# Optimization experiments

Hardware: AMD Instinct MI355X
Metric: run time of the kernel (lower is better)

The kernel has to match this reference:

```python
import jax, jax.numpy as jnp
import numpy as np

N_DET, N_MAP, N_PTS, C = 900, 100, 20, 256
IMG_W, IMG_H = 640.0, 480.0


def _grid_sample(feat, gx, gy):
    """Bilinear grid_sample, align_corners=False, zeros padding.
    feat: [C,H,W]; gx,gy: [N] normalized in [-1,1]. Returns [N,C]."""
    Cc, H, W = feat.shape
    x = (gx + 1.0) * (W * 0.5) - 0.5
    y = (gy + 1.0) * (H * 0.5) - 0.5
    x0 = jnp.floor(x); y0 = jnp.floor(y)
    wx1 = x - x0; wx0 = 1.0 - wx1
    wy1 = y - y0; wy0 = 1.0 - wy1

    def gather(xi, yi):
        inb = (xi >= 0) & (xi <= W - 1) & (yi >= 0) & (yi <= H - 1)
        xc = jnp.clip(xi, 0, W - 1).astype(jnp.int32)
        yc = jnp.clip(yi, 0, H - 1).astype(jnp.int32)
        return feat[:, yc, xc] * inb.astype(feat.dtype)  # [C,N]

    out = (gather(x0, y0) * (wx0 * wy0) + gather(x0 + 1, y0) * (wx1 * wy0)
           + gather(x0, y0 + 1) * (wx0 * wy1) + gather(x0 + 1, y0 + 1) * (wx1 * wy1))
    return out.T  # [N,C]


def _project(E, K, homo):
    """E:[6,4,4], K:[6,3,3], homo:[N,4] -> gx,gy,valid each [6,N]."""
    pc = jnp.einsum('cij,nj->cni', E, homo)            # [6,N,4]
    p2d = jnp.einsum('cij,cnj->cni', K, pc[..., :3])   # [6,N,3]
    depth = p2d[..., 2]
    u = p2d[..., 0] / (depth + 1e-6)
    v = p2d[..., 1] / (depth + 1e-6)
    valid = depth > 0.1
    gx = u / IMG_W * 2.0 - 1.0
    gy = v / IMG_H * 2.0 - 1.0
    return gx, gy, valid


def _sample_multiscale(feats, gx, gy, valid):
    """feats: list of [6,C,H,W]; gx,gy,valid: [6,N] -> [6,N,C]."""
    acc = None
    for f in feats:  # fixed 4 FPN levels
        s = jax.vmap(_grid_sample)(f, gx, gy)  # [6,N,C]
        acc = s if acc is None else acc + s
    acc = acc / len(feats)
    return acc * valid[..., None].astype(acc.dtype)


def setup_inputs():
    key = jax.random.key(0)
    ks = jax.random.split(key, 16)
    f = lambda i, shape, s=1.0: jax.random.normal(ks[i], shape, jnp.float32) * s
    p2 = f(0, (6, C, 120, 160))
    p3 = f(1, (6, C, 60, 80))
    p4 = f(2, (6, C, 30, 40))
    p5 = f(3, (6, C, 15, 20))
    K0 = jnp.array([[500.0, 0.0, 320.0], [0.0, 500.0, 240.0], [0.0, 0.0, 1.0]], jnp.float32)
    intrinsics = jnp.tile(K0, (6, 1, 1)) + f(4, (6, 3, 3), 0.5)
    extrinsics = jnp.tile(jnp.eye(4, dtype=jnp.float32), (6, 1, 1)) + f(5, (6, 4, 4), 0.3)
    det_anchors_3d = f(6, (N_DET, 3), 20.0)
    det_anchors_full = f(7, (N_DET, 11))
    map_anchors = f(8, (N_MAP, N_PTS, 2), 20.0)
    s = 1.0 / float(np.sqrt(C))
    return {
        'p2': p2, 'p3': p3, 'p4': p4, 'p5': p5,
        'intrinsics': intrinsics, 'extrinsics': extrinsics,
        'det_anchors_3d': det_anchors_3d, 'det_anchors_full': det_anchors_full,
        'map_anchors': map_anchors,
        'W1d': f(9, (C, C), s), 'b1d': jnp.zeros((C,), jnp.float32),
        'Wcd': f(10, (C, 4), s), 'bcd': jnp.zeros((4,), jnp.float32),
        'Wod': f(11, (C, 11), s), 'bod': jnp.zeros((11,), jnp.float32),
        'W1m': f(12, (C, C), s), 'b1m': jnp.zeros((C,), jnp.float32),
        'Wcm': f(13, (C, 3), s), 'bcm': jnp.zeros((3,), jnp.float32),
        'Wom': f(14, (C, N_PTS * 2), s), 'bom': jnp.zeros((N_PTS * 2,), jnp.float32),
    }


def reference(p2, p3, p4, p5, intrinsics, extrinsics, det_anchors_3d,
              det_anchors_full, map_anchors, W1d, b1d, Wcd, bcd, Wod, bod,
              W1m, b1m, Wcm, bcm, Wom, bom):
    feats = [p2, p3, p4, p5]
    ones_det = jnp.ones((N_DET, 1), det_anchors_3d.dtype)
    homo_det = jnp.concatenate([det_anchors_3d, ones_det], axis=-1)  # [900,4]
    centers = map_anchors.mean(axis=1)  # [100,2]
    homo_map = jnp.concatenate([centers,
                                jnp.zeros((N_MAP, 1), centers.dtype),
                                jnp.ones((N_MAP, 1), centers.dtype)], axis=-1)  # [100,4]

    gxd, gyd, vd = _project(extrinsics, intrinsics, homo_det)
    det_agg = _sample_multiscale(feats, gxd, gyd, vd).sum(0) / 6.0  # [900,256]
    gxm, gym, vm = _project(extrinsics, intrinsics, homo_map)
    map_agg = _sample_multiscale(feats, gxm, gym, vm).sum(0) / 6.0  # [100,256]

    hd = jax.nn.relu(det_agg @ W1d + b1d)
    det_classes = hd @ Wcd + bcd                     # [900,4]
    det_boxes = det_anchors_full + hd @ Wod + bod    # [900,11]
    hm = jax.nn.relu(map_agg @ W1m + b1m)
    map_classes = hm @ Wcm + bcm                     # [100,3]
    map_lines = map_anchors + (hm @ Wom + bom).reshape(N_MAP, N_PTS, 2)
    return det_classes, det_boxes, map_classes, map_lines
```

## Files before the change

### kernel.cpp

```cpp
#include <hip/hip_runtime.h>

#define CDIM 256
#define NDET 900
#define NMAP 100
#define NPTS 20
#define NBLK (NDET + NMAP)

#define P4OFF 7372800
#define P5OFF 9216000
#define ACCOFF 9292800
#define C3STR 1228800
#define C4STR 307200
#define C5STR 76800

__global__ __launch_bounds__(256, 4) void k1_pack_p2(
    const float* __restrict__ p2, const float* __restrict__ p3,
    const float* __restrict__ p4, const float* __restrict__ p5,
    const float* __restrict__ Kin, const float* __restrict__ Ein,
    const float* __restrict__ det3d, const float* __restrict__ mapanch,
    float* __restrict__ wsf)
{
    const int b = blockIdx.x;
    const int t = threadIdx.x;

    if (b < 630) {
        if (b < 360) {
            const int cam = b / 60, h = b % 60;
            const float4* __restrict__ src = (const float4*)(p3 + ((cam * CDIM + t) * 60 + h) * 80);
            float* __restrict__ dst = wsf + ((cam * 60 + h) * 80) * CDIM + t;
            #pragma unroll
            for (int w4 = 0; w4 < 20; ++w4) {
                const float4 v = src[w4];
                dst[(w4 * 4 + 0) * CDIM] = v.x;
                dst[(w4 * 4 + 1) * CDIM] = v.y;
                dst[(w4 * 4 + 2) * CDIM] = v.z;
                dst[(w4 * 4 + 3) * CDIM] = v.w;
            }
        } else if (b < 540) {
            const int bb = b - 360;
            const int cam = bb / 30, h = bb % 30;
            const float4* __restrict__ src = (const float4*)(p4 + ((cam * CDIM + t) * 30 + h) * 40);
            float* __restrict__ dst = wsf + P4OFF + ((cam * 30 + h) * 40) * CDIM + t;
            #pragma unroll
            for (int w4 = 0; w4 < 10; ++w4) {
                const float4 v = src[w4];
                dst[(w4 * 4 + 0) * CDIM] = v.x;
                dst[(w4 * 4 + 1) * CDIM] = v.y;
                dst[(w4 * 4 + 2) * CDIM] = v.z;
                dst[(w4 * 4 + 3) * CDIM] = v.w;
            }
        } else {
            const int bb = b - 540;
            const int cam = bb / 15, h = bb % 15;
            const float4* __restrict__ src = (const float4*)(p5 + ((cam * CDIM + t) * 15 + h) * 20);
            float* __restrict__ dst = wsf + P5OFF + ((cam * 15 + h) * 20) * CDIM + t;
            #pragma unroll
            for (int w4 = 0; w4 < 5; ++w4) {
                const float4 v = src[w4];
                dst[(w4 * 4 + 0) * CDIM] = v.x;
                dst[(w4 * 4 + 1) * CDIM] = v.y;
                dst[(w4 * 4 + 2) * CDIM] = v.z;
                dst[(w4 * 4 + 3) * CDIM] = v.w;
            }
        }
        return;
    }

    const int pt = b - 630;
    const bool isDet = (pt < NDET);
    const int m = pt - NDET;

    __shared__ int   s_off0[7][4];
    __shared__ float s_w0[7][4];
    __shared__ int   s_list0[8];
    __shared__ int   s_n0;

    if (t < 7) {
        float h0, h1, h2;
        if (isDet) {
            h0 = det3d[pt * 3 + 0];
            h1 = det3d[pt * 3 + 1];
            h2 = det3d[pt * 3 + 2];
        } else {
            float cx = 0.f, cy = 0.f;
            #pragma unroll
            for (int j = 0; j < NPTS; ++j) {
                cx += mapanch[(m * NPTS + j) * 2 + 0];
                cy += mapanch[(m * NPTS + j) * 2 + 1];
            }
            h0 = cx / (float)NPTS;
            h1 = cy / (float)NPTS;
            h2 = 0.f;
        }

        bool pred = false;
        if (t < 6) {
            const int cam = t;
            float pc[3];
            #pragma unroll
            for (int i = 0; i < 3; ++i) {
                pc[i] = Ein[cam * 16 + i * 4 + 0] * h0
                      + Ein[cam * 16 + i * 4 + 1] * h1
                      + Ein[cam * 16 + i * 4 + 2] * h2
                      + Ein[cam * 16 + i * 4 + 3] * 1.f;
            }
            const float q0 = Kin[cam*9+0]*pc[0] + Kin[cam*9+1]*pc[1] + Kin[cam*9+2]*pc[2];
            const float q1 = Kin[cam*9+3]*pc[0] + Kin[cam*9+4]*pc[1] + Kin[cam*9+5]*pc[2];
            const float q2 = Kin[cam*9+6]*pc[0] + Kin[cam*9+7]*pc[1] + Kin[cam*9+8]*pc[2];
            const float depth = q2;
            const float u = q0 / (depth + 1e-6f);
            const float v = q1 / (depth + 1e-6f);
            const bool valid = (depth > 0.1f);
            const float gx = u / 640.0f * 2.0f - 1.0f;
            const float gy = v / 480.0f * 2.0f - 1.0f;

            const int H = 120, W = 160;
            const float x = (gx + 1.f) * (W * 0.5f) - 0.5f;
            const float y = (gy + 1.f) * (H * 0.5f) - 0.5f;
            const float x0f = floorf(x), y0f = floorf(y);
            const float wx1 = x - x0f, wx0 = 1.f - wx1;
            const float wy1 = y - y0f, wy0 = 1.f - wy1;
            const float x1f = x0f + 1.f, y1f = y0f + 1.f;
            const bool bx0 = (x0f >= 0.f) && (x0f <= (float)(W - 1));
            const bool bx1 = (x1f >= 0.f) && (x1f <= (float)(W - 1));
            const bool by0 = (y0f >= 0.f) && (y0f <= (float)(H - 1));
            const bool by1 = (y1f >= 0.f) && (y1f <= (float)(H - 1));
            const int xc0 = (int)fminf(fmaxf(x0f, 0.f), (float)(W - 1));
            const int xc1 = (int)fminf(fmaxf(x1f, 0.f), (float)(W - 1));
            const int yc0 = (int)fminf(fmaxf(y0f, 0.f), (float)(H - 1));
            const int yc1 = (int)fminf(fmaxf(y1f, 0.f), (float)(H - 1));
            const int base = cam * CDIM * H * W;
            s_off0[t][0] = base + yc0 * W + xc0;
            s_off0[t][1] = base + yc0 * W + xc1;
            s_off0[t][2] = base + yc1 * W + xc0;
            s_off0[t][3] = base + yc1 * W + xc1;
            const float w0 = (bx0 && by0) ? wx0 * wy0 : 0.f;
            const float w1 = (bx1 && by0) ? wx1 * wy0 : 0.f;
            const float w2 = (bx0 && by1) ? wx0 * wy1 : 0.f;
            const float w3 = (bx1 && by1) ? wx1 * wy1 : 0.f;
            s_w0[t][0] = w0; s_w0[t][1] = w1; s_w0[t][2] = w2; s_w0[t][3] = w3;
            pred = valid && ((w0 + w1 + w2 + w3) != 0.f);
        } else {
            s_off0[6][0] = 0; s_off0[6][1] = 0; s_off0[6][2] = 0; s_off0[6][3] = 0;
            s_w0[6][0] = 0.f; s_w0[6][1] = 0.f; s_w0[6][2] = 0.f; s_w0[6][3] = 0.f;
        }
        const unsigned long long mask = __ballot(pred);
        const int n = __popcll(mask);
        const int rank = __popcll(mask & ((1ull << t) - 1ull));
        if (pred) s_list0[rank] = t;
        const int npad = (n + 1) & ~1;
        if (t < 2 && (n + t) < npad) s_list0[n + t] = 6;
        if (t == 0) s_n0 = npad;
    }
    __syncthreads();

    float acc = 0.f;
    const int npad = s_n0;
    const int cHW = t * 19200;
    for (int base = 0; base < npad; base += 2) {
        float v[2][4];
        int tj[2];
        #pragma unroll
        for (int j = 0; j < 2; ++j) {
            const int tt = s_list0[base + j];
            tj[j] = tt;
            v[j][0] = p2[s_off0[tt][0] + cHW];
            v[j][1] = p2[s_off0[tt][1] + cHW];
            v[j][2] = p2[s_off0[tt][2] + cHW];
            v[j][3] = p2[s_off0[tt][3] + cHW];
        }
        #pragma unroll
        for (int j = 0; j < 2; ++j) {
            const int tt = tj[j];
            acc += s_w0[tt][0] * v[j][0] + s_w0[tt][1] * v[j][1]
                 + s_w0[tt][2] * v[j][2] + s_w0[tt][3] * v[j][3];
        }
    }
    wsf[ACCOFF + pt * CDIM + t] = acc;
}

__global__ __launch_bounds__(256, 4) void k2_gather_mlp(
    const float* __restrict__ wsf,
    const float* __restrict__ Kin, const float* __restrict__ Ein,
    const float* __restrict__ det3d, const float* __restrict__ detfull,
    const float* __restrict__ mapanch,
    const float* __restrict__ W1d, const float* __restrict__ b1d,
    const float* __restrict__ Wcd, const float* __restrict__ bcd,
    const float* __restrict__ Wod, const float* __restrict__ bod,
    const float* __restrict__ W1m, const float* __restrict__ b1m,
    const float* __restrict__ Wcm, const float* __restrict__ bcm,
    const float* __restrict__ Wom, const float* __restrict__ bom,
    float* __restrict__ out)
{
    const int pt = blockIdx.x;
    const int t  = threadIdx.x;
    const bool isDet = (pt < NDET);
    const int m = pt - NDET;

    __shared__ int   s_off[19][4];
    __shared__ float s_w[19][4];
    __shared__ int   s_list[24];
    __shared__ int   s_n;
    __shared__ float s_vec[CDIM];
    __shared__ float s_hid[CDIM];

    float acc = wsf[ACCOFF + pt * CDIM + t];

    if (t < 19) {
        float h0, h1, h2;
        if (isDet) {
            h0 = det3d[pt * 3 + 0];
            h1 = det3d[pt * 3 + 1];
            h2 = det3d[pt * 3 + 2];
        } else {
            float cx = 0.f, cy = 0.f;
            #pragma unroll
            for (int j = 0; j < NPTS; ++j) {
                cx += mapanch[(m * NPTS + j) * 2 + 0];
                cy += mapanch[(m * NPTS + j) * 2 + 1];
            }
            h0 = cx / (float)NPTS;
            h1 = cy / (float)NPTS;
            h2 = 0.f;
        }

        bool pred = false;
        if (t < 18) {
            const int cam = t / 3, l = 1 + (t % 3);
            float pc[3];
            #pragma unroll
            for (int i = 0; i < 3; ++i) {
                pc[i] = Ein[cam * 16 + i * 4 + 0] * h0
                      + Ein[cam * 16 + i * 4 + 1] * h1
                      + Ein[cam * 16 + i * 4 + 2] * h2
                      + Ein[cam * 16 + i * 4 + 3] * 1.f;
            }
            const float q0 = Kin[cam*9+0]*pc[0] + Kin[cam*9+1]*pc[1] + Kin[cam*9+2]*pc[2];
            const float q1 = Kin[cam*9+3]*pc[0] + Kin[cam*9+4]*pc[1] + Kin[cam*9+5]*pc[2];
            const float q2 = Kin[cam*9+6]*pc[0] + Kin[cam*9+7]*pc[1] + Kin[cam*9+8]*pc[2];
            const float depth = q2;
            const float u = q0 / (depth + 1e-6f);
            const float v = q1 / (depth + 1e-6f);
            const bool valid = (depth > 0.1f);
            const float gx = u / 640.0f * 2.0f - 1.0f;
            const float gy = v / 480.0f * 2.0f - 1.0f;

            const int Hs[4] = {120, 60, 30, 15};
            const int Ws[4] = {160, 80, 40, 20};
            const int H = Hs[l], W = Ws[l];
            const float x = (gx + 1.f) * (W * 0.5f) - 0.5f;
            const float y = (gy + 1.f) * (H * 0.5f) - 0.5f;
            const float x0f = floorf(x), y0f = floorf(y);
            const float wx1 = x - x0f, wx0 = 1.f - wx1;
            const float wy1 = y - y0f, wy0 = 1.f - wy1;
            const float x1f = x0f + 1.f, y1f = y0f + 1.f;
            const bool bx0 = (x0f >= 0.f) && (x0f <= (float)(W - 1));
            const bool bx1 = (x1f >= 0.f) && (x1f <= (float)(W - 1));
            const bool by0 = (y0f >= 0.f) && (y0f <= (float)(H - 1));
            const bool by1 = (y1f >= 0.f) && (y1f <= (float)(H - 1));
            const int xc0 = (int)fminf(fmaxf(x0f, 0.f), (float)(W - 1));
            const int xc1 = (int)fminf(fmaxf(x1f, 0.f), (float)(W - 1));
            const int yc0 = (int)fminf(fmaxf(y0f, 0.f), (float)(H - 1));
            const int yc1 = (int)fminf(fmaxf(y1f, 0.f), (float)(H - 1));
            const int pb = (l == 1) ? cam * C3STR
                         : (l == 2) ? (P4OFF + cam * C4STR)
                                    : (P5OFF + cam * C5STR);
            s_off[t][0] = pb + (yc0 * W + xc0) * CDIM;
            s_off[t][1] = pb + (yc0 * W + xc1) * CDIM;
            s_off[t][2] = pb + (yc1 * W + xc0) * CDIM;
            s_off[t][3] = pb + (yc1 * W + xc1) * CDIM;
            const float w0 = (bx0 && by0) ? wx0 * wy0 : 0.f;
            const float w1 = (bx1 && by0) ? wx1 * wy0 : 0.f;
            const float w2 = (bx0 && by1) ? wx0 * wy1 : 0.f;
            const float w3 = (bx1 && by1) ? wx1 * wy1 : 0.f;
            s_w[t][0] = w0; s_w[t][1] = w1; s_w[t][2] = w2; s_w[t][3] = w3;
            pred = valid && ((w0 + w1 + w2 + w3) != 0.f);
        } else {
            s_off[18][0] = 0; s_off[18][1] = 0; s_off[18][2] = 0; s_off[18][3] = 0;
            s_w[18][0] = 0.f; s_w[18][1] = 0.f; s_w[18][2] = 0.f; s_w[18][3] = 0.f;
        }

        const unsigned long long mask = __ballot(pred);
        const int n = __popcll(mask);
        const int rank = __popcll(mask & ((1ull << t) - 1ull));
        if (pred) s_list[rank] = t;
        const int npad = (n + 7) & ~7;
        if (t < 8 && (n + t) < npad) s_list[n + t] = 18;
        if (t == 0) s_n = npad;
    }
    __syncthreads();

    const int npad = s_n;
    for (int base = 0; base < npad; base += 8) {
        float v[8][4];
        int tj[8];
        #pragma unroll
        for (int j = 0; j < 8; ++j) {
            const int tt = s_list[base + j];
            tj[j] = tt;
            v[j][0] = wsf[s_off[tt][0] + t];
            v[j][1] = wsf[s_off[tt][1] + t];
            v[j][2] = wsf[s_off[tt][2] + t];
            v[j][3] = wsf[s_off[tt][3] + t];
        }
        #pragma unroll
        for (int j = 0; j < 8; ++j) {
            const int tt = tj[j];
            acc += s_w[tt][0] * v[j][0] + s_w[tt][1] * v[j][1]
                 + s_w[tt][2] * v[j][2] + s_w[tt][3] * v[j][3];
        }
    }
    const float agg = (acc * 0.25f) / 6.0f;

    s_vec[t] = agg;
    __syncthreads();

    const float* __restrict__ W1 = isDet ? W1d : W1m;
    const float* __restrict__ b1 = isDet ? b1d : b1m;
    float hsum = b1[t];
    const float4* sv4 = (const float4*)s_vec;
    float wvA[32], wvB[32];
    #pragma unroll
    for (int i = 0; i < 32; ++i) wvA[i] = W1[i * CDIM + t];
    #pragma unroll
    for (int k0 = 0; k0 < CDIM; k0 += 64) {
        #pragma unroll
        for (int i = 0; i < 32; ++i) wvB[i] = W1[(k0 + 32 + i) * CDIM + t];
        #pragma unroll
        for (int i = 0; i < 8; ++i) {
            const float4 x = sv4[(k0 >> 2) + i];
            hsum = fmaf(x.x, wvA[4 * i + 0], hsum);
            hsum = fmaf(x.y, wvA[4 * i + 1], hsum);
            hsum = fmaf(x.z, wvA[4 * i + 2], hsum);
            hsum = fmaf(x.w, wvA[4 * i + 3], hsum);
        }
        if (k0 + 64 < CDIM) {
            #pragma unroll
            for (int i = 0; i < 32; ++i) wvA[i] = W1[(k0 + 64 + i) * CDIM + t];
        }
        #pragma unroll
        for (int i = 0; i < 8; ++i) {
            const float4 x = sv4[(k0 >> 2) + 8 + i];
            hsum = fmaf(x.x, wvB[4 * i + 0], hsum);
            hsum = fmaf(x.y, wvB[4 * i + 1], hsum);
            hsum = fmaf(x.z, wvB[4 * i + 2], hsum);
            hsum = fmaf(x.w, wvB[4 * i + 3], hsum);
        }
    }
    s_hid[t] = fmaxf(hsum, 0.f);
    __syncthreads();

    const int g  = t >> 4;
    const int ln = t & 15;
    const int nOut = isDet ? 15 : 43;
    const int nrep = isDet ? 1 : 3;
    for (int rep = 0; rep < nrep; ++rep) {
        const int o = g + rep * 16;
        if (o < nOut) {
            const float* Wp; int stride, oo, ooff; float bias;
            if (isDet) {
                if (o < 4) { Wp = Wcd; stride = 4;  oo = o;     ooff = pt * 4 + oo;         bias = bcd[oo]; }
                else       { Wp = Wod; stride = 11; oo = o - 4; ooff = 3600 + pt * 11 + oo; bias = bod[oo] + detfull[pt * 11 + oo]; }
            } else {
                if (o < 3) { Wp = Wcm; stride = 3;  oo = o;     ooff = 13500 + m * 3 + oo;  bias = bcm[oo]; }
                else       { Wp = Wom; stride = 40; oo = o - 3; ooff = 13800 + m * 40 + oo; bias = bom[oo] + mapanch[m * 40 + oo]; }
            }
            float wv[16], xv[16];
            #pragma unroll
            for (int kk = 0; kk < 16; ++kk) wv[kk] = Wp[(ln + kk * 16) * stride + oo];
            #pragma unroll
            for (int kk = 0; kk < 16; ++kk) xv[kk] = s_hid[ln + kk * 16];
            float sp = 0.f;
            #pragma unroll
            for (int kk = 0; kk < 16; ++kk) sp = fmaf(xv[kk], wv[kk], sp);
            #pragma unroll
            for (int off = 1; off < 16; off <<= 1) sp += __shfl_xor(sp, off, 64);
            if (ln == 0) out[ooff] = sp + bias;
        }
    }
}

extern "C" void kernel_launch(void* const* d_in, const int* in_sizes, int n_in,
                              void* d_out, int out_size, void* d_ws, size_t ws_size,
                              hipStream_t stream) {
    const float* p2      = (const float*)d_in[0];
    const float* p3      = (const float*)d_in[1];
    const float* p4      = (const float*)d_in[2];
    const float* p5      = (const float*)d_in[3];
    const float* Kin     = (const float*)d_in[4];
    const float* Ein     = (const float*)d_in[5];
    const float* det3d   = (const float*)d_in[6];
    const float* detfull = (const float*)d_in[7];
    const float* mapanch = (const float*)d_in[8];
    const float* W1d     = (const float*)d_in[9];
    const float* b1d     = (const float*)d_in[10];
    const float* Wcd     = (const float*)d_in[11];
    const float* bcd     = (const float*)d_in[12];
    const float* Wod     = (const float*)d_in[13];
    const float* bod     = (const float*)d_in[14];
    const float* W1m     = (const float*)d_in[15];
    const float* b1m     = (const float*)d_in[16];
    const float* Wcm     = (const float*)d_in[17];
    const float* bcm     = (const float*)d_in[18];
    const float* Wom     = (const float*)d_in[19];
    const float* bom     = (const float*)d_in[20];
    float* out = (float*)d_out;
    float* wsf = (float*)d_ws;

    k1_pack_p2<<<1630, 256, 0, stream>>>(
        p2, p3, p4, p5, Kin, Ein, det3d, mapanch, wsf);

    k2_gather_mlp<<<NBLK, 256, 0, stream>>>(
        wsf, Kin, Ein, det3d, detfull, mapanch,
        W1d, b1d, Wcd, bcd, Wod, bod, W1m, b1m, Wcm, bcm, Wom, bom, out);
}
```

Measured before the change: 52.45 us.

## Store transposed FPN levels as bf16 and use LDS-tiled transpose for p3

The channel-last repack of p3/p4/p5 now writes bf16 instead of fp32, halving workspace write traffic and the later gather reads in the second kernel. The p3 repack switches from per-row strided scatter to a 64x64 shared-memory tiled transpose, so both global reads and writes are coalesced. The grid grows to 3070 blocks. The cost is reduced precision on three of the four pyramid levels, which may move outputs against the fp32 reference.

```diff
diff --git a/kernel.cpp b/kernel.cpp
--- a/kernel.cpp
+++ b/kernel.cpp
@@ -6,67 +6,86 @@
 #define NPTS 20
 #define NBLK (NDET + NMAP)
 
-#define P4OFF 7372800
-#define P5OFF 9216000
-#define ACCOFF 9292800
+using u16 = unsigned short;
+
+#define U4OFF 7372800
+#define U5OFF 9216000
+#define UEND  9676800
+#define ACCF  4838400
 #define C3STR 1228800
 #define C4STR 307200
 #define C5STR 76800
+
+__device__ __forceinline__ u16 f2bf(float f) {
+    union { float f; unsigned int i; } v; v.f = f;
+    return (u16)((v.i + 0x7FFFu + ((v.i >> 16) & 1u)) >> 16);
+}
+__device__ __forceinline__ float bf2f(u16 u) {
+    union { unsigned int i; float f; } v; v.i = ((unsigned int)u) << 16; return v.f;
+}
 
 __global__ __launch_bounds__(256, 4) void k1_pack_p2(
     const float* __restrict__ p2, const float* __restrict__ p3,
     const float* __restrict__ p4, const float* __restrict__ p5,
     const float* __restrict__ Kin, const float* __restrict__ Ein,
     const float* __restrict__ det3d, const float* __restrict__ mapanch,
-    float* __restrict__ wsf)
+    u16* __restrict__ wsb, float* __restrict__ accw)
 {
     const int b = blockIdx.x;
     const int t = threadIdx.x;
 
-    if (b < 630) {
-        if (b < 360) {
-            const int cam = b / 60, h = b % 60;
-            const float4* __restrict__ src = (const float4*)(p3 + ((cam * CDIM + t) * 60 + h) * 80);
-            float* __restrict__ dst = wsf + ((cam * 60 + h) * 80) * CDIM + t;
-            #pragma unroll
-            for (int w4 = 0; w4 < 20; ++w4) {
-                const float4 v = src[w4];
-                dst[(w4 * 4 + 0) * CDIM] = v.x;
-                dst[(w4 * 4 + 1) * CDIM] = v.y;
-                dst[(w4 * 4 + 2) * CDIM] = v.z;
-                dst[(w4 * 4 + 3) * CDIM] = v.w;
-            }
-        } else if (b < 540) {
-            const int bb = b - 360;
-            const int cam = bb / 30, h = bb % 30;
-            const float4* __restrict__ src = (const float4*)(p4 + ((cam * CDIM + t) * 30 + h) * 40);
-            float* __restrict__ dst = wsf + P4OFF + ((cam * 30 + h) * 40) * CDIM + t;
-            #pragma unroll
-            for (int w4 = 0; w4 < 10; ++w4) {
-                const float4 v = src[w4];
-                dst[(w4 * 4 + 0) * CDIM] = v.x;
-                dst[(w4 * 4 + 1) * CDIM] = v.y;
-                dst[(w4 * 4 + 2) * CDIM] = v.z;
-                dst[(w4 * 4 + 3) * CDIM] = v.w;
-            }
-        } else {
-            const int bb = b - 540;
-            const int cam = bb / 15, h = bb % 15;
-            const float4* __restrict__ src = (const float4*)(p5 + ((cam * CDIM + t) * 15 + h) * 20);
-            float* __restrict__ dst = wsf + P5OFF + ((cam * 15 + h) * 20) * CDIM + t;
-            #pragma unroll
-            for (int w4 = 0; w4 < 5; ++w4) {
-                const float4 v = src[w4];
-                dst[(w4 * 4 + 0) * CDIM] = v.x;
-                dst[(w4 * 4 + 1) * CDIM] = v.y;
-                dst[(w4 * 4 + 2) * CDIM] = v.z;
-                dst[(w4 * 4 + 3) * CDIM] = v.w;
-            }
+    __shared__ float s_tile[64][65];
+
+    if (b < 1800) {
+        const int cam = b / 300;
+        const int rem = b % 300;
+        const int pxT = rem >> 2, chT = rem & 3;
+        const int lane = t & 63, wv = t >> 6;
+        #pragma unroll
+        for (int cc = 0; cc < 16; ++cc) {
+            const int chl = wv * 16 + cc;
+            s_tile[chl][lane] = p3[(cam * CDIM + chT * 64 + chl) * 4800 + pxT * 64 + lane];
+        }
+        __syncthreads();
+        #pragma unroll
+        for (int pp = 0; pp < 16; ++pp) {
+            const int pxl = wv * 16 + pp;
+            wsb[(cam * 4800 + pxT * 64 + pxl) * CDIM + chT * 64 + lane] = f2bf(s_tile[lane][pxl]);
         }
         return;
     }
-
-    const int pt = b - 630;
+    if (b < 1980) {
+        const int id = b - 1800;
+        const int cam = id / 30, h = id % 30;
+        const float4* __restrict__ src = (const float4*)(p4 + ((cam * CDIM + t) * 30 + h) * 40);
+        u16* __restrict__ dst = wsb + U4OFF + ((cam * 30 + h) * 40) * CDIM + t;
+        #pragma unroll
+        for (int w4 = 0; w4 < 10; ++w4) {
+            const float4 v = src[w4];
+            dst[(w4 * 4 + 0) * CDIM] = f2bf(v.x);
+            dst[(w4 * 4 + 1) * CDIM] = f2bf(v.y);
+            dst[(w4 * 4 + 2) * CDIM] = f2bf(v.z);
+            dst[(w4 * 4 + 3) * CDIM] = f2bf(v.w);
+        }
+        return;
+    }
+    if (b < 2070) {
+        const int id = b - 1980;
+        const int cam = id / 15, h = id % 15;
+        const float4* __restrict__ src = (const float4*)(p5 + ((cam * CDIM + t) * 15 + h) * 20);
+        u16* __restrict__ dst = wsb + U5OFF + ((cam * 15 + h) * 20) * CDIM + t;
+        #pragma unroll
+        for (int w4 = 0; w4 < 5; ++w4) {
+            const float4 v = src[w4];
+            dst[(w4 * 4 + 0) * CDIM] = f2bf(v.x);
+            dst[(w4 * 4 + 1) * CDIM] = f2bf(v.y);
+            dst[(w4 * 4 + 2) * CDIM] = f2bf(v.z);
+            dst[(w4 * 4 + 3) * CDIM] = f2bf(v.w);
+        }
+        return;
+    }
+
+    const int pt = b - 2070;
     const bool isDet = (pt < NDET);
     const int m = pt - NDET;
 
@@ -88,11 +107,8 @@
                 cx += mapanch[(m * NPTS + j) * 2 + 0];
                 cy += mapanch[(m * NPTS + j) * 2 + 1];
             }
-            h0 = cx / (float)NPTS;
-            h1 = cy / (float)NPTS;
-            h2 = 0.f;
-        }
-
+            h0 = cx / (float)NPTS; h1 = cy / (float)NPTS; h2 = 0.f;
+        }
         bool pred = false;
         if (t < 6) {
             const int cam = t;
@@ -113,7 +129,6 @@
             const bool valid = (depth > 0.1f);
             const float gx = u / 640.0f * 2.0f - 1.0f;
             const float gy = v / 480.0f * 2.0f - 1.0f;
-
             const int H = 120, W = 160;
             const float x = (gx + 1.f) * (W * 0.5f) - 0.5f;
             const float y = (gy + 1.f) * (H * 0.5f) - 0.5f;
@@ -176,11 +191,11 @@
                  + s_w0[tt][2] * v[j][2] + s_w0[tt][3] * v[j][3];
         }
     }
-    wsf[ACCOFF + pt * CDIM + t] = acc;
+    accw[pt * CDIM + t] = acc;
 }
 
 __global__ __launch_bounds__(256, 4) void k2_gather_mlp(
-    const float* __restrict__ wsf,
+    const u16* __restrict__ wsb, const float* __restrict__ accw,
     const float* __restrict__ Kin, const float* __restrict__ Ein,
     const float* __restrict__ det3d, const float* __restrict__ detfull,
     const float* __restrict__ mapanch,
@@ -204,7 +219,7 @@
     __shared__ float s_vec[CDIM];
     __shared__ float s_hid[CDIM];
 
-    float acc = wsf[ACCOFF + pt * CDIM + t];
+    float acc = accw[pt * CDIM + t];
 
     if (t < 19) {
         float h0, h1, h2;
@@ -219,11 +234,8 @@
                 cx += mapanch[(m * NPTS + j) * 2 + 0];
                 cy += mapanch[(m * NPTS + j) * 2 + 1];
             }
-            h0 = cx / (float)NPTS;
-            h1 = cy / (float)NPTS;
-            h2 = 0.f;
-        }
-
+            h0 = cx / (float)NPTS; h1 = cy / (float)NPTS; h2 = 0.f;
+        }
         bool pred = false;
         if (t < 18) {
             const int cam = t / 3, l = 1 + (t % 3);
@@ -244,7 +256,6 @@
             const bool valid = (depth > 0.1f);
             const float gx = u / 640.0f * 2.0f - 1.0f;
             const float gy = v / 480.0f * 2.0f - 1.0f;
-
             const int Hs[4] = {120, 60, 30, 15};
             const int Ws[4] = {160, 80, 40, 20};
             const int H = Hs[l], W = Ws[l];
@@ -263,8 +274,8 @@
             const int yc0 = (int)fminf(fmaxf(y0f, 0.f), (float)(H - 1));
             const int yc1 = (int)fminf(fmaxf(y1f, 0.f), (float)(H - 1));
             const int pb = (l == 1) ? cam * C3STR
-                         : (l == 2) ? (P4OFF + cam * C4STR)
-                                    : (P5OFF + cam * C5STR);
+                         : (l == 2) ? (U4OFF + cam * C4STR)
+                                    : (U5OFF + cam * C5STR);
             s_off[t][0] = pb + (yc0 * W + xc0) * CDIM;
             s_off[t][1] = pb + (yc0 * W + xc1) * CDIM;
             s_off[t][2] = pb + (yc1 * W + xc0) * CDIM;
@@ -279,7 +290,6 @@
             s_off[18][0] = 0; s_off[18][1] = 0; s_off[18][2] = 0; s_off[18][3] = 0;
             s_w[18][0] = 0.f; s_w[18][1] = 0.f; s_w[18][2] = 0.f; s_w[18][3] = 0.f;
         }
-
         const unsigned long long mask = __ballot(pred);
         const int n = __popcll(mask);
         const int rank = __popcll(mask & ((1ull << t) - 1ull));
@@ -298,10 +308,10 @@
         for (int j = 0; j < 8; ++j) {
             const int tt = s_list[base + j];
             tj[j] = tt;
-            v[j][0] = wsf[s_off[tt][0] + t];
-            v[j][1] = wsf[s_off[tt][1] + t];
-            v[j][2] = wsf[s_off[tt][2] + t];
-            v[j][3] = wsf[s_off[tt][3] + t];
+            v[j][0] = bf2f(wsb[s_off[tt][0] + t]);
+            v[j][1] = bf2f(wsb[s_off[tt][1] + t]);
+            v[j][2] = bf2f(wsb[s_off[tt][2] + t]);
+            v[j][3] = bf2f(wsb[s_off[tt][3] + t]);
         }
         #pragma unroll
         for (int j = 0; j < 8; ++j) {
@@ -405,12 +415,13 @@
     const float* Wom     = (const float*)d_in[19];
     const float* bom     = (const float*)d_in[20];
     float* out = (float*)d_out;
-    float* wsf = (float*)d_ws;
-
-    k1_pack_p2<<<1630, 256, 0, stream>>>(
-        p2, p3, p4, p5, Kin, Ein, det3d, mapanch, wsf);
+    u16* wsb = (u16*)d_ws;
+    float* accw = (float*)d_ws + ACCF;
+
+    k1_pack_p2<<<3070, 256, 0, stream>>>(
+        p2, p3, p4, p5, Kin, Ein, det3d, mapanch, wsb, accw);
 
     k2_gather_mlp<<<NBLK, 256, 0, stream>>>(
-        wsf, Kin, Ein, det3d, detfull, mapanch,
+        wsb, accw, Kin, Ein, det3d, detfull, mapanch,
         W1d, b1d, Wcd, bcd, Wod, bod, W1m, b1m, Wcm, bcm, Wom, bom, out);
 }
```

Result: faster. 51.02 us (-2.7%).
